# Kernel optimization log

Measured on AMD Instinct MI355X. Metric: run time of the kernel, lower is better.

## Reference

```python
import jax, jax.numpy as jnp
import numpy as np

V, D, H, L = 32000, 1024, 1024, 2
B, S = 64, 256

def setup_inputs() -> dict:
    key = jax.random.key(0)
    k_emb, k_wx, k_wh, k_in, k_len = jax.random.split(key, 5)
    sc = 1.0 / np.sqrt(H)
    embedding = jax.random.normal(k_emb, (V, D), dtype=jnp.float32) * sc
    Wx = jax.random.normal(k_wx, (L, D, 4 * H), dtype=jnp.float32) * sc  # layer input kernels (D==H)
    Wh = jax.random.normal(k_wh, (L, H, 4 * H), dtype=jnp.float32) * sc  # recurrent kernels
    b = jnp.zeros((L, 4 * H), dtype=jnp.float32).at[:, H:2 * H].set(1.0)  # forget-gate bias = 1
    inputs = jax.random.randint(k_in, (B, S), 0, V)
    lengths = jax.random.randint(k_len, (B,), 1, S + 1)
    return {"inputs": inputs, "lengths": lengths, "train": 1,
            "embedding": embedding, "Wx": Wx, "Wh": Wh, "b": b}

def _lstm_layer(x, lengths, Wx, Wh, b):
    # x: [B, S, D]; masked update freezes (c, h) once t >= length (state after EOS).
    Bn, Sn, _ = x.shape
    Hn = Wh.shape[0]
    c0 = jnp.zeros((Bn, Hn), x.dtype)
    h0 = jnp.zeros((Bn, Hn), x.dtype)
    xg = jnp.einsum('bsd,dg->sbg', x, Wx) + b  # precompute input projections [S,B,4H]

    def step(carry, inp):
        c, h, t = carry
        gates = inp + h @ Wh  # [B, 4H]
        i, f, g, o = jnp.split(gates, 4, axis=-1)
        c_new = jax.nn.sigmoid(f) * c + jax.nn.sigmoid(i) * jnp.tanh(g)
        h_new = jax.nn.sigmoid(o) * jnp.tanh(c_new)
        mask = (t < lengths)[:, None]
        c = jnp.where(mask, c_new, c)
        h = jnp.where(mask, h_new, h)
        return (c, h, t + 1), h

    (c_f, h_f, _), hs = jax.lax.scan(step, (c0, h0, jnp.int32(0)), xg)
    return jnp.transpose(hs, (1, 0, 2)), c_f, h_f  # [B,S,H], [B,H], [B,H]

def reference(inputs, lengths, train, embedding, Wx, Wh, b):
    # embed (dropout rates are 0 -> identity)
    x = embedding[inputs]  # [B, S, D]
    cs, hs = [], []
    for l in range(Wx.shape[0]):
        x, c_f, h_f = _lstm_layer(x, lengths, Wx[l], Wh[l], b[l])
        cs.append(c_f)
        hs.append(h_f)
    return x, (jnp.stack(cs), jnp.stack(hs))  # outputs, per-layer final (c, h)
```

## Files before the change

### kernel.cpp

```cpp
#include <hip/hip_runtime.h>
#include <cstdint>
#include <cstddef>

#define VV  32000
#define DD  1024
#define HH  1024
#define LL  2
#define BB  64
#define SS  256
#define G4  4096

typedef __attribute__((ext_vector_type(8))) short short8;
typedef __attribute__((ext_vector_type(4))) float f32x4;
typedef unsigned short u16;
typedef unsigned int u32;

__device__ __forceinline__ u16 f2bf(float f) {
  union { float f; u32 u; } v; v.f = f;
  u32 u = v.u + 0x7fffu + ((v.u >> 16) & 1u);
  return (u16)(u >> 16);
}
__device__ __forceinline__ float bf2f(u16 b) {
  union { u32 u; float f; } v; v.u = ((u32)b) << 16;
  return v.f;
}
__device__ __forceinline__ float sigm(float x) { return 1.f / (1.f + __expf(-x)); }
__device__ __forceinline__ float tanh_fast(float x) {
  return 1.f - 2.f / (__expf(2.f * x) + 1.f);
}

__global__ void embed_kernel(const int* __restrict__ inputs,
                             const float* __restrict__ emb,
                             u16* __restrict__ x0) {
  int m = blockIdx.x;
  int s = m >> 6, b = m & 63;
  int tok = inputs[b * SS + s];
  const f32x4* src = (const f32x4*)(emb + (size_t)tok * DD);
  f32x4 v = src[threadIdx.x];
  u32 lo = (u32)f2bf(v[0]) | ((u32)f2bf(v[1]) << 16);
  u32 hi = (u32)f2bf(v[2]) | ((u32)f2bf(v[3]) << 16);
  u32* dst = (u32*)(x0 + (size_t)m * DD + threadIdx.x * 4);
  dst[0] = lo; dst[1] = hi;
}

__global__ void permW_kernel(const float* __restrict__ Wx, const float* __restrict__ Wh,
                             u16* __restrict__ WxPT, u16* __restrict__ WhPT) {
  __shared__ float tl[64][65];
  int bid = blockIdx.x;
  int which = bid >> 10;
  int tile = bid & 1023;
  int ktile = tile >> 6, ntile = tile & 63;
  const float* src = ((which < 2) ? Wx : Wh) + (size_t)(which & 1) * G4 * 1024;
  u16* dst = ((which < 2) ? WxPT : WhPT) + (size_t)(which & 1) * G4 * 1024;
  int tid = threadIdx.x;
  #pragma unroll
  for (int i = 0; i < 16; ++i) {
    int idx = i * 256 + tid;
    int kk = idx >> 6, nn = idx & 63;
    tl[kk][nn] = src[(size_t)(ktile * 64 + kk) * G4 + ntile * 64 + nn];
  }
  __syncthreads();
  #pragma unroll
  for (int i = 0; i < 16; ++i) {
    int idx = i * 256 + tid;
    int nn = idx >> 6, kk = idx & 63;
    int n = ntile * 64 + nn;
    int p = ((n & 1023) << 2) | (n >> 10);
    dst[(size_t)p * 1024 + ktile * 64 + kk] = f2bf(tl[kk][nn]);
  }
}

__global__ void permB_kernel(const float* __restrict__ bb, float* __restrict__ bP) {
  int idx = blockIdx.x * 256 + threadIdx.x;
  int l = idx >> 12, p = idx & 4095;
  int h = p >> 2, g = p & 3;
  bP[idx] = bb[l * G4 + g * 1024 + h];
}

__device__ __forceinline__ void gld_lds16(const void* g, void* l) {
  __builtin_amdgcn_global_load_lds((const __attribute__((address_space(1))) unsigned int*)g,
                                   (__attribute__((address_space(3))) unsigned int*)l, 16, 0, 0);
}

__global__ __launch_bounds__(256) void gemm_xg(
    const u16* __restrict__ A, const u16* __restrict__ W,
    const float* __restrict__ bP, float* Cf, u16* Cb, int out_f32) {
  __shared__ u16 As[128 * 32];
  __shared__ u16 Bs[128 * 32];
  const int tid = threadIdx.x;
  const int wave = tid >> 6, lane = tid & 63;
  const int bid = blockIdx.x;
  const int nt = bid & 31, mt = bid >> 5;
  const u16* Ap = A + (size_t)mt * 128 * 1024;
  const u16* Wp = W + (size_t)nt * 128 * 1024;
  f32x4 acc[4][4];
  #pragma unroll
  for (int i = 0; i < 4; ++i)
    #pragma unroll
    for (int j = 0; j < 4; ++j) acc[i][j] = (f32x4){0.f, 0.f, 0.f, 0.f};
  const int wm = wave >> 1, wn = wave & 1;
  const int r16 = lane & 15, oct = lane >> 4;
  for (int k0 = 0; k0 < 1024; k0 += 32) {
    #pragma unroll
    for (int issue = 0; issue < 2; ++issue) {
      int cb = issue * 256 + wave * 64;
      int c = cb + lane;
      gld_lds16(Ap + (size_t)(c >> 2) * 1024 + k0 + (c & 3) * 8, As + (size_t)cb * 8);
      gld_lds16(Wp + (size_t)(c >> 2) * 1024 + k0 + (c & 3) * 8, Bs + (size_t)cb * 8);
    }
    asm volatile("s_waitcnt vmcnt(0)" ::: "memory");
    __syncthreads();
    short8 af[4], bfr[4];
    #pragma unroll
    for (int i = 0; i < 4; ++i)
      af[i] = *(const short8*)(As + (wm * 64 + i * 16 + r16) * 32 + oct * 8);
    #pragma unroll
    for (int j = 0; j < 4; ++j)
      bfr[j] = *(const short8*)(Bs + (wn * 64 + j * 16 + r16) * 32 + oct * 8);
    #pragma unroll
    for (int i = 0; i < 4; ++i)
      #pragma unroll
      for (int j = 0; j < 4; ++j)
        acc[i][j] = __builtin_amdgcn_mfma_f32_16x16x32_bf16(af[i], bfr[j], acc[i][j], 0, 0, 0);
    __syncthreads();
  }
  #pragma unroll
  for (int j = 0; j < 4; ++j) {
    int n = nt * 128 + wn * 64 + j * 16 + r16;
    float bias = bP[n];
    #pragma unroll
    for (int i = 0; i < 4; ++i) {
      int m = mt * 128 + wm * 64 + i * 16 + oct * 4;
      #pragma unroll
      for (int r = 0; r < 4; ++r) {
        float val = acc[i][j][r] + bias;
        if (out_f32) Cf[(size_t)(m + r) * G4 + n] = val;
        else         Cb[(size_t)(m + r) * G4 + n] = f2bf(val);
      }
    }
  }
}

__global__ __launch_bounds__(256, 1) void recur_kernel(
    const u16* __restrict__ WhPT,
    const float* xgf, const u16* xgb, int xg_f32,
    const int* __restrict__ lengths,
    u16* __restrict__ hbuf,
    u16* __restrict__ hs_out,
    float* __restrict__ x_out,
    float* __restrict__ c_out, float* __restrict__ h_out,
    int layer, int* flags) {
  __shared__ u16 hA[16][1032];
  __shared__ float gbuf[16][64];
  __shared__ float xgbuf[16][64];
  __shared__ int len_s[16];
  const int tid = threadIdx.x;
  const int wave = tid >> 6, lane = tid & 63;
  const int bg = blockIdx.x >> 6, cg = blockIdx.x & 63;
  const int r16 = lane & 15, oct = lane >> 4;

  short8 bfrag[32];
  {
    const u16* wrow = WhPT + (size_t)(cg * 64 + wave * 16 + r16) * 1024 + oct * 8;
    #pragma unroll
    for (int kk = 0; kk < 32; ++kk) bfrag[kk] = *(const short8*)(wrow + kk * 32);
    #pragma unroll
    for (int kk = 0; kk < 32; ++kk) asm volatile("" : "+a"(bfrag[kk]));
  }
  if (tid < 16) len_s[tid] = lengths[bg * 16 + tid];
  const int b_loc = tid >> 4, hc_loc = tid & 15;
  const int b_glob = bg * 16 + b_loc;
  const int hc_glob = cg * 16 + hc_loc;
  float c_reg = 0.f, h_reg = 0.f;
  if (!(tid & 1))
    __hip_atomic_store((u32*)(hbuf + (size_t)b_glob * 1024 + hc_glob), 0u,
                       __ATOMIC_RELAXED, __HIP_MEMORY_SCOPE_AGENT);

  int* myflags = flags + bg * 64;
  f32x4 xg_next;
  {
    size_t xrow = (size_t)(0 * 64 + b_glob) * G4 + cg * 64 + hc_loc * 4;
    if (xg_f32) xg_next = *(const f32x4*)(xgf + xrow);
    else {
      const u16* s = xgb + xrow;
      f32x4 v; v[0] = bf2f(s[0]); v[1] = bf2f(s[1]); v[2] = bf2f(s[2]); v[3] = bf2f(s[3]);
      xg_next = v;
    }
  }

  for (int t = 0; t < SS; ++t) {
    __syncthreads();
    if (tid == 0)
      __hip_atomic_store(&myflags[cg], t + 1, __ATOMIC_RELAXED, __HIP_MEMORY_SCOPE_AGENT);
    if (wave == 0) {
      while (__hip_atomic_load(&myflags[lane], __ATOMIC_RELAXED, __HIP_MEMORY_SCOPE_AGENT) < t + 1)
        __builtin_amdgcn_s_sleep(1);
    }
    __syncthreads();
    {
      const u16* hsrc = hbuf + (size_t)(t & 1) * (BB * 1024) + (size_t)b_glob * 1024;
      unsigned long long addr = (unsigned long long)(hsrc + hc_loc * 8);
      short8 v0, v1, v2, v3, v4, v5, v6, v7;
      asm volatile(
        "global_load_dwordx4 %0, %8, off sc1\n\t"
        "global_load_dwordx4 %1, %8, off offset:256 sc1\n\t"
        "global_load_dwordx4 %2, %8, off offset:512 sc1\n\t"
        "global_load_dwordx4 %3, %8, off offset:768 sc1\n\t"
        "global_load_dwordx4 %4, %8, off offset:1024 sc1\n\t"
        "global_load_dwordx4 %5, %8, off offset:1280 sc1\n\t"
        "global_load_dwordx4 %6, %8, off offset:1536 sc1\n\t"
        "global_load_dwordx4 %7, %8, off offset:1792 sc1\n\t"
        "s_waitcnt vmcnt(0)"
        : "=v"(v0), "=v"(v1), "=v"(v2), "=v"(v3),
          "=v"(v4), "=v"(v5), "=v"(v6), "=v"(v7)
        : "v"(addr) : "memory");
      *(short8*)(&hA[b_loc][(hc_loc +   0) * 8]) = v0;
      *(short8*)(&hA[b_loc][(hc_loc +  16) * 8]) = v1;
      *(short8*)(&hA[b_loc][(hc_loc +  32) * 8]) = v2;
      *(short8*)(&hA[b_loc][(hc_loc +  48) * 8]) = v3;
      *(short8*)(&hA[b_loc][(hc_loc +  64) * 8]) = v4;
      *(short8*)(&hA[b_loc][(hc_loc +  80) * 8]) = v5;
      *(short8*)(&hA[b_loc][(hc_loc +  96) * 8]) = v6;
      *(short8*)(&hA[b_loc][(hc_loc + 112) * 8]) = v7;
      *(f32x4*)(&xgbuf[b_loc][hc_loc * 4]) = xg_next;
      if (t + 1 < SS) {
        size_t xrow = (size_t)((t + 1) * 64 + b_glob) * G4 + cg * 64 + hc_loc * 4;
        if (xg_f32) xg_next = *(const f32x4*)(xgf + xrow);
        else {
          const u16* s = xgb + xrow;
          f32x4 v; v[0] = bf2f(s[0]); v[1] = bf2f(s[1]); v[2] = bf2f(s[2]); v[3] = bf2f(s[3]);
          xg_next = v;
        }
      }
    }
    __syncthreads();
    f32x4 acc0 = (f32x4){0.f, 0.f, 0.f, 0.f};
    f32x4 acc1 = (f32x4){0.f, 0.f, 0.f, 0.f};
    #pragma unroll
    for (int kk = 0; kk < 16; ++kk) {
      short8 a0 = *(const short8*)(&hA[r16][(2 * kk) * 32 + oct * 8]);
      short8 a1 = *(const short8*)(&hA[r16][(2 * kk + 1) * 32 + oct * 8]);
      acc0 = __builtin_amdgcn_mfma_f32_16x16x32_bf16(a0, bfrag[2 * kk], acc0, 0, 0, 0);
      acc1 = __builtin_amdgcn_mfma_f32_16x16x32_bf16(a1, bfrag[2 * kk + 1], acc1, 0, 0, 0);
    }
    f32x4 acc = acc0 + acc1;
    #pragma unroll
    for (int r = 0; r < 4; ++r) gbuf[oct * 4 + r][wave * 16 + r16] = acc[r];
    __syncthreads();
    f32x4 g = *(const f32x4*)(&gbuf[b_loc][hc_loc * 4]);
    f32x4 xv = *(const f32x4*)(&xgbuf[b_loc][hc_loc * 4]);
    float si = sigm(g[0] + xv[0]);
    float sf = sigm(g[1] + xv[1]);
    float gg = tanh_fast(g[2] + xv[2]);
    float so = sigm(g[3] + xv[3]);
    float c_new = sf * c_reg + si * gg;
    float h_new = so * tanh_fast(c_new);
    if (t < len_s[b_loc]) { c_reg = c_new; h_reg = h_new; }
    u32 hb = (u32)f2bf(h_reg);
    u32 nb = (u32)__shfl_xor((int)hb, 1);
    u32 packed = hb | (nb << 16);
    if (!(tid & 1))
      __hip_atomic_store((u32*)(hbuf + (size_t)((t + 1) & 1) * (BB * 1024) +
                                (size_t)b_glob * 1024 + hc_glob),
                         packed, __ATOMIC_RELAXED, __HIP_MEMORY_SCOPE_AGENT);
    if (layer == 0) {
      if (!(tid & 1))
        __builtin_nontemporal_store(packed,
            (u32*)(hs_out + (size_t)(t * 64 + b_glob) * 1024 + hc_glob));
    } else {
      __builtin_nontemporal_store(h_reg,
          x_out + (size_t)(b_glob * SS + t) * 1024 + hc_glob);
    }
  }
  c_out[(size_t)b_glob * 1024 + hc_glob] = c_reg;
  h_out[(size_t)b_glob * 1024 + hc_glob] = h_reg;
}

extern "C" void kernel_launch(void* const* d_in, const int* in_sizes, int n_in,
                              void* d_out, int out_size, void* d_ws, size_t ws_size,
                              hipStream_t stream) {
  const int* inputs  = (const int*)d_in[0];
  const int* lengths = (const int*)d_in[1];
  const float* emb   = (const float*)d_in[3];
  const float* Wx    = (const float*)d_in[4];
  const float* Wh    = (const float*)d_in[5];
  const float* bb    = (const float*)d_in[6];
  float* out = (float*)d_out;

  char* ws = (char*)d_ws;
  size_t off = 0;
  auto alloc = [&](size_t bytes) -> void* {
    void* p = ws + off;
    off = (off + bytes + 255) & ~(size_t)255;
    return p;
  };
  u16* WxPT = (u16*)alloc((size_t)2 * G4 * 1024 * 2);
  u16* WhPT = (u16*)alloc((size_t)2 * G4 * 1024 * 2);
  float* bP = (float*)alloc((size_t)2 * G4 * 4);
  u16* x0   = (u16*)alloc((size_t)16384 * 1024 * 2);
  u16* hs0  = (u16*)alloc((size_t)16384 * 1024 * 2);
  u16* hbuf = (u16*)alloc((size_t)2 * BB * 1024 * 2);
  int* flags = (int*)alloc(2048);
  size_t xg_f32_bytes = (size_t)16384 * G4 * 4;
  int xg_f32 = (ws_size > off) && ((ws_size - off) >= xg_f32_bytes);
  float* xgf = (float*)(ws + off);
  u16* xgb   = (u16*)(ws + off);

  hipMemsetAsync(flags, 0, 2048, stream);
  embed_kernel<<<dim3(16384), dim3(256), 0, stream>>>(inputs, emb, x0);
  permW_kernel<<<dim3(4096), dim3(256), 0, stream>>>(Wx, Wh, WxPT, WhPT);
  permB_kernel<<<dim3(32), dim3(256), 0, stream>>>(bb, bP);

  float* cs_base = out + (size_t)BB * SS * HH;
  float* hs_base = cs_base + (size_t)LL * BB * HH;

  for (int layer = 0; layer < 2; ++layer) {
    const u16* Aten = (layer == 0) ? x0 : hs0;
    gemm_xg<<<dim3(4096), dim3(256), 0, stream>>>(
        Aten, WxPT + (size_t)layer * G4 * 1024, bP + layer * G4, xgf, xgb, xg_f32);
    const u16* Whl = WhPT + (size_t)layer * G4 * 1024;
    float* c_out_p = cs_base + (size_t)layer * BB * HH;
    float* h_out_p = hs_base + (size_t)layer * BB * HH;
    int* flags_l = flags + layer * 256;
    const float* xgf_c = xgf; const u16* xgb_c = xgb;
    void* args[] = { (void*)&Whl, (void*)&xgf_c, (void*)&xgb_c, (void*)&xg_f32,
                     (void*)&lengths, (void*)&hbuf, (void*)&hs0, (void*)&out,
                     (void*)&c_out_p, (void*)&h_out_p, (void*)&layer,
                     (void*)&flags_l };
    hipLaunchCooperativeKernel((void*)recur_kernel, dim3(256), dim3(256), args, 0, stream);
  }
}
```

Before: 2.765 ms.

## Fuse both LSTM layers into one wavefront-pipelined recurrent kernel

Replaces the two sequential per-layer recurrent kernels, and the layer-1 input-projection GEMM, with one cooperative kernel of 512 threads per block. Waves 0-3 run layer 0 at step s while waves 4-7 run layer 1 at step s-1. Layer 1 computes its input projection on the fly from the layer-0 hidden state, using register-resident Wx1 and Wh1 fragments. This removes one full grid-synchronised sequence of 256 steps, the layer-1 xg GEMM and the hs0 round trip through memory. The cost is double the register pressure for weight fragments, extra MFMA work per step on the layer-1 waves, and one extra step in the pipeline.

```diff
diff --git a/kernel.cpp b/kernel.cpp
--- a/kernel.cpp
+++ b/kernel.cpp
@@ -141,45 +141,89 @@
   }
 }
 
-__global__ __launch_bounds__(256, 1) void recur_kernel(
-    const u16* __restrict__ WhPT,
+#define STAGE_TILE(HSRC, HADST) do {                                          \
+    unsigned long long addr_ = (unsigned long long)((HSRC) + hc_loc * 8);     \
+    short8 v0, v1, v2, v3, v4, v5, v6, v7;                                    \
+    asm volatile(                                                             \
+      "global_load_dwordx4 %0, %8, off sc1\n\t"                               \
+      "global_load_dwordx4 %1, %8, off offset:256 sc1\n\t"                    \
+      "global_load_dwordx4 %2, %8, off offset:512 sc1\n\t"                    \
+      "global_load_dwordx4 %3, %8, off offset:768 sc1\n\t"                    \
+      "global_load_dwordx4 %4, %8, off offset:1024 sc1\n\t"                   \
+      "global_load_dwordx4 %5, %8, off offset:1280 sc1\n\t"                   \
+      "global_load_dwordx4 %6, %8, off offset:1536 sc1\n\t"                   \
+      "global_load_dwordx4 %7, %8, off offset:1792 sc1\n\t"                   \
+      "s_waitcnt vmcnt(0)"                                                    \
+      : "=v"(v0), "=v"(v1), "=v"(v2), "=v"(v3),                               \
+        "=v"(v4), "=v"(v5), "=v"(v6), "=v"(v7)                                \
+      : "v"(addr_) : "memory");                                               \
+    *(short8*)(&(HADST)[b_loc][(hc_loc +   0) * 8]) = v0;                     \
+    *(short8*)(&(HADST)[b_loc][(hc_loc +  16) * 8]) = v1;                     \
+    *(short8*)(&(HADST)[b_loc][(hc_loc +  32) * 8]) = v2;                     \
+    *(short8*)(&(HADST)[b_loc][(hc_loc +  48) * 8]) = v3;                     \
+    *(short8*)(&(HADST)[b_loc][(hc_loc +  64) * 8]) = v4;                     \
+    *(short8*)(&(HADST)[b_loc][(hc_loc +  80) * 8]) = v5;                     \
+    *(short8*)(&(HADST)[b_loc][(hc_loc +  96) * 8]) = v6;                     \
+    *(short8*)(&(HADST)[b_loc][(hc_loc + 112) * 8]) = v7;                     \
+  } while (0)
+
+__global__ __launch_bounds__(512, 1) void recur2_kernel(
+    const u16* __restrict__ Wh0PT,
+    const u16* __restrict__ Wx1PT,
+    const u16* __restrict__ Wh1PT,
     const float* xgf, const u16* xgb, int xg_f32,
+    const float* __restrict__ b1P,
     const int* __restrict__ lengths,
-    u16* __restrict__ hbuf,
-    u16* __restrict__ hs_out,
+    u16* __restrict__ h0buf,
+    u16* __restrict__ h1buf,
     float* __restrict__ x_out,
-    float* __restrict__ c_out, float* __restrict__ h_out,
-    int layer, int* flags) {
-  __shared__ u16 hA[16][1032];
-  __shared__ float gbuf[16][64];
+    float* __restrict__ c0_out, float* __restrict__ h0_out,
+    float* __restrict__ c1_out, float* __restrict__ h1_out,
+    int* flags) {
+  __shared__ u16 hA0[16][1032];
+  __shared__ u16 hA1[16][1032];
+  __shared__ float gbuf0[16][64];
+  __shared__ float gbuf1[16][64];
   __shared__ float xgbuf[16][64];
   __shared__ int len_s[16];
   const int tid = threadIdx.x;
   const int wave = tid >> 6, lane = tid & 63;
   const int bg = blockIdx.x >> 6, cg = blockIdx.x & 63;
   const int r16 = lane & 15, oct = lane >> 4;
-
-  short8 bfrag[32];
+  const bool lo = (wave < 4);
+  const int wv = wave & 3;
+
+  short8 bfA[32], bfB[32];
   {
-    const u16* wrow = WhPT + (size_t)(cg * 64 + wave * 16 + r16) * 1024 + oct * 8;
-    #pragma unroll
-    for (int kk = 0; kk < 32; ++kk) bfrag[kk] = *(const short8*)(wrow + kk * 32);
-    #pragma unroll
-    for (int kk = 0; kk < 32; ++kk) asm volatile("" : "+a"(bfrag[kk]));
+    const u16* rowA = (lo ? Wh0PT : Wx1PT) + (size_t)(cg * 64 + wv * 16 + r16) * 1024 + oct * 8;
+    const u16* rowB = (lo ? Wh0PT : Wh1PT) + (size_t)(cg * 64 + wv * 16 + r16) * 1024 + oct * 8;
+    #pragma unroll
+    for (int kk = 0; kk < 32; ++kk) bfA[kk] = *(const short8*)(rowA + kk * 32);
+    #pragma unroll
+    for (int kk = 0; kk < 32; ++kk) asm volatile("" : "+a"(bfA[kk]));
+    #pragma unroll
+    for (int kk = 0; kk < 32; ++kk) bfB[kk] = *(const short8*)(rowB + kk * 32);
+    #pragma unroll
+    for (int kk = 0; kk < 32; ++kk) asm volatile("" : "+a"(bfB[kk]));
   }
   if (tid < 16) len_s[tid] = lengths[bg * 16 + tid];
-  const int b_loc = tid >> 4, hc_loc = tid & 15;
+  const int th = tid & 255;
+  const int b_loc = th >> 4, hc_loc = th & 15;
   const int b_glob = bg * 16 + b_loc;
   const int hc_glob = cg * 16 + hc_loc;
   float c_reg = 0.f, h_reg = 0.f;
-  if (!(tid & 1))
-    __hip_atomic_store((u32*)(hbuf + (size_t)b_glob * 1024 + hc_glob), 0u,
+  if (!(tid & 1)) {
+    u16* zb = lo ? h0buf : h1buf;
+    __hip_atomic_store((u32*)(zb + (size_t)b_glob * 1024 + hc_glob), 0u,
                        __ATOMIC_RELAXED, __HIP_MEMORY_SCOPE_AGENT);
+  }
+  f32x4 bias1 = (f32x4){0.f, 0.f, 0.f, 0.f};
+  if (!lo) bias1 = *(const f32x4*)(b1P + hc_glob * 4);
 
   int* myflags = flags + bg * 64;
-  f32x4 xg_next;
-  {
-    size_t xrow = (size_t)(0 * 64 + b_glob) * G4 + cg * 64 + hc_loc * 4;
+  f32x4 xg_next = (f32x4){0.f, 0.f, 0.f, 0.f};
+  if (lo) {
+    size_t xrow = (size_t)b_glob * G4 + cg * 64 + hc_loc * 4;
     if (xg_f32) xg_next = *(const f32x4*)(xgf + xrow);
     else {
       const u16* s = xgb + xrow;
@@ -188,92 +232,115 @@
     }
   }
 
-  for (int t = 0; t < SS; ++t) {
+  for (int s = 0; s <= SS; ++s) {
     __syncthreads();
     if (tid == 0)
-      __hip_atomic_store(&myflags[cg], t + 1, __ATOMIC_RELAXED, __HIP_MEMORY_SCOPE_AGENT);
+      __hip_atomic_store(&myflags[cg], s + 1, __ATOMIC_RELAXED, __HIP_MEMORY_SCOPE_AGENT);
     if (wave == 0) {
-      while (__hip_atomic_load(&myflags[lane], __ATOMIC_RELAXED, __HIP_MEMORY_SCOPE_AGENT) < t + 1)
+      while (__hip_atomic_load(&myflags[lane], __ATOMIC_RELAXED, __HIP_MEMORY_SCOPE_AGENT) < s + 1)
         __builtin_amdgcn_s_sleep(1);
     }
     __syncthreads();
-    {
-      const u16* hsrc = hbuf + (size_t)(t & 1) * (BB * 1024) + (size_t)b_glob * 1024;
-      unsigned long long addr = (unsigned long long)(hsrc + hc_loc * 8);
-      short8 v0, v1, v2, v3, v4, v5, v6, v7;
-      asm volatile(
-        "global_load_dwordx4 %0, %8, off sc1\n\t"
-        "global_load_dwordx4 %1, %8, off offset:256 sc1\n\t"
-        "global_load_dwordx4 %2, %8, off offset:512 sc1\n\t"
-        "global_load_dwordx4 %3, %8, off offset:768 sc1\n\t"
-        "global_load_dwordx4 %4, %8, off offset:1024 sc1\n\t"
-        "global_load_dwordx4 %5, %8, off offset:1280 sc1\n\t"
-        "global_load_dwordx4 %6, %8, off offset:1536 sc1\n\t"
-        "global_load_dwordx4 %7, %8, off offset:1792 sc1\n\t"
-        "s_waitcnt vmcnt(0)"
-        : "=v"(v0), "=v"(v1), "=v"(v2), "=v"(v3),
-          "=v"(v4), "=v"(v5), "=v"(v6), "=v"(v7)
-        : "v"(addr) : "memory");
-      *(short8*)(&hA[b_loc][(hc_loc +   0) * 8]) = v0;
-      *(short8*)(&hA[b_loc][(hc_loc +  16) * 8]) = v1;
-      *(short8*)(&hA[b_loc][(hc_loc +  32) * 8]) = v2;
-      *(short8*)(&hA[b_loc][(hc_loc +  48) * 8]) = v3;
-      *(short8*)(&hA[b_loc][(hc_loc +  64) * 8]) = v4;
-      *(short8*)(&hA[b_loc][(hc_loc +  80) * 8]) = v5;
-      *(short8*)(&hA[b_loc][(hc_loc +  96) * 8]) = v6;
-      *(short8*)(&hA[b_loc][(hc_loc + 112) * 8]) = v7;
+    if (lo) {
+      const u16* hsrc = h0buf + (size_t)(s & 1) * (BB * 1024) + (size_t)b_glob * 1024;
+      STAGE_TILE(hsrc, hA0);
       *(f32x4*)(&xgbuf[b_loc][hc_loc * 4]) = xg_next;
-      if (t + 1 < SS) {
-        size_t xrow = (size_t)((t + 1) * 64 + b_glob) * G4 + cg * 64 + hc_loc * 4;
+      if (s + 1 < SS) {
+        size_t xrow = (size_t)((s + 1) * 64 + b_glob) * G4 + cg * 64 + hc_loc * 4;
         if (xg_f32) xg_next = *(const f32x4*)(xgf + xrow);
         else {
-          const u16* s = xgb + xrow;
-          f32x4 v; v[0] = bf2f(s[0]); v[1] = bf2f(s[1]); v[2] = bf2f(s[2]); v[3] = bf2f(s[3]);
+          const u16* sp = xgb + xrow;
+          f32x4 v; v[0] = bf2f(sp[0]); v[1] = bf2f(sp[1]); v[2] = bf2f(sp[2]); v[3] = bf2f(sp[3]);
           xg_next = v;
         }
       }
-    }
-    __syncthreads();
-    f32x4 acc0 = (f32x4){0.f, 0.f, 0.f, 0.f};
-    f32x4 acc1 = (f32x4){0.f, 0.f, 0.f, 0.f};
-    #pragma unroll
-    for (int kk = 0; kk < 16; ++kk) {
-      short8 a0 = *(const short8*)(&hA[r16][(2 * kk) * 32 + oct * 8]);
-      short8 a1 = *(const short8*)(&hA[r16][(2 * kk + 1) * 32 + oct * 8]);
-      acc0 = __builtin_amdgcn_mfma_f32_16x16x32_bf16(a0, bfrag[2 * kk], acc0, 0, 0, 0);
-      acc1 = __builtin_amdgcn_mfma_f32_16x16x32_bf16(a1, bfrag[2 * kk + 1], acc1, 0, 0, 0);
-    }
-    f32x4 acc = acc0 + acc1;
-    #pragma unroll
-    for (int r = 0; r < 4; ++r) gbuf[oct * 4 + r][wave * 16 + r16] = acc[r];
-    __syncthreads();
-    f32x4 g = *(const f32x4*)(&gbuf[b_loc][hc_loc * 4]);
-    f32x4 xv = *(const f32x4*)(&xgbuf[b_loc][hc_loc * 4]);
-    float si = sigm(g[0] + xv[0]);
-    float sf = sigm(g[1] + xv[1]);
-    float gg = tanh_fast(g[2] + xv[2]);
-    float so = sigm(g[3] + xv[3]);
-    float c_new = sf * c_reg + si * gg;
-    float h_new = so * tanh_fast(c_new);
-    if (t < len_s[b_loc]) { c_reg = c_new; h_reg = h_new; }
-    u32 hb = (u32)f2bf(h_reg);
-    u32 nb = (u32)__shfl_xor((int)hb, 1);
-    u32 packed = hb | (nb << 16);
-    if (!(tid & 1))
-      __hip_atomic_store((u32*)(hbuf + (size_t)((t + 1) & 1) * (BB * 1024) +
-                                (size_t)b_glob * 1024 + hc_glob),
-                         packed, __ATOMIC_RELAXED, __HIP_MEMORY_SCOPE_AGENT);
-    if (layer == 0) {
+    } else if (s >= 1) {
+      const u16* hsrc = h1buf + (size_t)((s - 1) & 1) * (BB * 1024) + (size_t)b_glob * 1024;
+      STAGE_TILE(hsrc, hA1);
+    }
+    __syncthreads();
+    if (lo) {
+      if (s < SS) {
+        f32x4 acc0 = (f32x4){0.f, 0.f, 0.f, 0.f};
+        f32x4 acc1 = (f32x4){0.f, 0.f, 0.f, 0.f};
+        #pragma unroll
+        for (int kk = 0; kk < 16; ++kk) {
+          short8 a0 = *(const short8*)(&hA0[r16][(2 * kk) * 32 + oct * 8]);
+          short8 a1 = *(const short8*)(&hA0[r16][(2 * kk + 1) * 32 + oct * 8]);
+          acc0 = __builtin_amdgcn_mfma_f32_16x16x32_bf16(a0, bfA[2 * kk], acc0, 0, 0, 0);
+          acc1 = __builtin_amdgcn_mfma_f32_16x16x32_bf16(a1, bfA[2 * kk + 1], acc1, 0, 0, 0);
+        }
+        f32x4 acc = acc0 + acc1;
+        #pragma unroll
+        for (int r = 0; r < 4; ++r) gbuf0[oct * 4 + r][wv * 16 + r16] = acc[r];
+      }
+    } else if (s >= 1) {
+      f32x4 ax0 = (f32x4){0.f, 0.f, 0.f, 0.f};
+      f32x4 ax1 = (f32x4){0.f, 0.f, 0.f, 0.f};
+      f32x4 ah0 = (f32x4){0.f, 0.f, 0.f, 0.f};
+      f32x4 ah1 = (f32x4){0.f, 0.f, 0.f, 0.f};
+      #pragma unroll
+      for (int kk = 0; kk < 16; ++kk) {
+        short8 a0 = *(const short8*)(&hA0[r16][(2 * kk) * 32 + oct * 8]);
+        short8 a1 = *(const short8*)(&hA0[r16][(2 * kk + 1) * 32 + oct * 8]);
+        short8 c0 = *(const short8*)(&hA1[r16][(2 * kk) * 32 + oct * 8]);
+        short8 c1 = *(const short8*)(&hA1[r16][(2 * kk + 1) * 32 + oct * 8]);
+        ax0 = __builtin_amdgcn_mfma_f32_16x16x32_bf16(a0, bfA[2 * kk], ax0, 0, 0, 0);
+        ax1 = __builtin_amdgcn_mfma_f32_16x16x32_bf16(a1, bfA[2 * kk + 1], ax1, 0, 0, 0);
+        ah0 = __builtin_amdgcn_mfma_f32_16x16x32_bf16(c0, bfB[2 * kk], ah0, 0, 0, 0);
+        ah1 = __builtin_amdgcn_mfma_f32_16x16x32_bf16(c1, bfB[2 * kk + 1], ah1, 0, 0, 0);
+      }
+      f32x4 acc = (ax0 + ax1) + (ah0 + ah1);
+      #pragma unroll
+      for (int r = 0; r < 4; ++r) gbuf1[oct * 4 + r][wv * 16 + r16] = acc[r];
+    }
+    __syncthreads();
+    if (lo) {
+      if (s < SS) {
+        f32x4 g = *(const f32x4*)(&gbuf0[b_loc][hc_loc * 4]);
+        f32x4 xv = *(const f32x4*)(&xgbuf[b_loc][hc_loc * 4]);
+        float si = sigm(g[0] + xv[0]);
+        float sf = sigm(g[1] + xv[1]);
+        float gg = tanh_fast(g[2] + xv[2]);
+        float so = sigm(g[3] + xv[3]);
+        float c_new = sf * c_reg + si * gg;
+        float h_new = so * tanh_fast(c_new);
+        if (s < len_s[b_loc]) { c_reg = c_new; h_reg = h_new; }
+        u32 hb = (u32)f2bf(h_reg);
+        u32 nb = (u32)__shfl_xor((int)hb, 1);
+        u32 packed = hb | (nb << 16);
+        if (!(tid & 1))
+          __hip_atomic_store((u32*)(h0buf + (size_t)((s + 1) & 1) * (BB * 1024) +
+                                    (size_t)b_glob * 1024 + hc_glob),
+                             packed, __ATOMIC_RELAXED, __HIP_MEMORY_SCOPE_AGENT);
+      }
+    } else if (s >= 1) {
+      f32x4 g = *(const f32x4*)(&gbuf1[b_loc][hc_loc * 4]);
+      float si = sigm(g[0] + bias1[0]);
+      float sf = sigm(g[1] + bias1[1]);
+      float gg = tanh_fast(g[2] + bias1[2]);
+      float so = sigm(g[3] + bias1[3]);
+      float c_new = sf * c_reg + si * gg;
+      float h_new = so * tanh_fast(c_new);
+      if (s - 1 < len_s[b_loc]) { c_reg = c_new; h_reg = h_new; }
+      u32 hb = (u32)f2bf(h_reg);
+      u32 nb = (u32)__shfl_xor((int)hb, 1);
+      u32 packed = hb | (nb << 16);
       if (!(tid & 1))
-        __builtin_nontemporal_store(packed,
-            (u32*)(hs_out + (size_t)(t * 64 + b_glob) * 1024 + hc_glob));
-    } else {
+        __hip_atomic_store((u32*)(h1buf + (size_t)(s & 1) * (BB * 1024) +
+                                  (size_t)b_glob * 1024 + hc_glob),
+                           packed, __ATOMIC_RELAXED, __HIP_MEMORY_SCOPE_AGENT);
       __builtin_nontemporal_store(h_reg,
-          x_out + (size_t)(b_glob * SS + t) * 1024 + hc_glob);
-    }
-  }
-  c_out[(size_t)b_glob * 1024 + hc_glob] = c_reg;
-  h_out[(size_t)b_glob * 1024 + hc_glob] = h_reg;
+          x_out + (size_t)(b_glob * SS + (s - 1)) * 1024 + hc_glob);
+    }
+  }
+  if (lo) {
+    c0_out[(size_t)b_glob * 1024 + hc_glob] = c_reg;
+    h0_out[(size_t)b_glob * 1024 + hc_glob] = h_reg;
+  } else {
+    c1_out[(size_t)b_glob * 1024 + hc_glob] = c_reg;
+    h1_out[(size_t)b_glob * 1024 + hc_glob] = h_reg;
+  }
 }
 
 extern "C" void kernel_launch(void* const* d_in, const int* in_sizes, int n_in,
@@ -298,35 +365,40 @@
   u16* WhPT = (u16*)alloc((size_t)2 * G4 * 1024 * 2);
   float* bP = (float*)alloc((size_t)2 * G4 * 4);
   u16* x0   = (u16*)alloc((size_t)16384 * 1024 * 2);
-  u16* hs0  = (u16*)alloc((size_t)16384 * 1024 * 2);
-  u16* hbuf = (u16*)alloc((size_t)2 * BB * 1024 * 2);
-  int* flags = (int*)alloc(2048);
+  u16* h0buf = (u16*)alloc((size_t)2 * BB * 1024 * 2);
+  u16* h1buf = (u16*)alloc((size_t)2 * BB * 1024 * 2);
+  int* flags = (int*)alloc(1024);
   size_t xg_f32_bytes = (size_t)16384 * G4 * 4;
   int xg_f32 = (ws_size > off) && ((ws_size - off) >= xg_f32_bytes);
   float* xgf = (float*)(ws + off);
   u16* xgb   = (u16*)(ws + off);
 
-  hipMemsetAsync(flags, 0, 2048, stream);
+  hipMemsetAsync(flags, 0, 1024, stream);
   embed_kernel<<<dim3(16384), dim3(256), 0, stream>>>(inputs, emb, x0);
   permW_kernel<<<dim3(4096), dim3(256), 0, stream>>>(Wx, Wh, WxPT, WhPT);
   permB_kernel<<<dim3(32), dim3(256), 0, stream>>>(bb, bP);
 
+  gemm_xg<<<dim3(4096), dim3(256), 0, stream>>>(x0, WxPT, bP, xgf, xgb, xg_f32);
+
   float* cs_base = out + (size_t)BB * SS * HH;
   float* hs_base = cs_base + (size_t)LL * BB * HH;
 
-  for (int layer = 0; layer < 2; ++layer) {
-    const u16* Aten = (layer == 0) ? x0 : hs0;
-    gemm_xg<<<dim3(4096), dim3(256), 0, stream>>>(
-        Aten, WxPT + (size_t)layer * G4 * 1024, bP + layer * G4, xgf, xgb, xg_f32);
-    const u16* Whl = WhPT + (size_t)layer * G4 * 1024;
-    float* c_out_p = cs_base + (size_t)layer * BB * HH;
-    float* h_out_p = hs_base + (size_t)layer * BB * HH;
-    int* flags_l = flags + layer * 256;
-    const float* xgf_c = xgf; const u16* xgb_c = xgb;
-    void* args[] = { (void*)&Whl, (void*)&xgf_c, (void*)&xgb_c, (void*)&xg_f32,
-                     (void*)&lengths, (void*)&hbuf, (void*)&hs0, (void*)&out,
-                     (void*)&c_out_p, (void*)&h_out_p, (void*)&layer,
-                     (void*)&flags_l };
-    hipLaunchCooperativeKernel((void*)recur_kernel, dim3(256), dim3(256), args, 0, stream);
-  }
-}
+  const u16* Wh0 = WhPT;
+  const u16* Wx1 = WxPT + (size_t)G4 * 1024;
+  const u16* Wh1 = WhPT + (size_t)G4 * 1024;
+  const float* b1 = bP + G4;
+  const float* xgf_c = xgf;
+  const u16* xgb_c = xgb;
+  float* c0_out = cs_base;
+  float* c1_out = cs_base + (size_t)BB * HH;
+  float* h0_out = hs_base;
+  float* h1_out = hs_base + (size_t)BB * HH;
+  void* args[] = { (void*)&Wh0, (void*)&Wx1, (void*)&Wh1,
+                   (void*)&xgf_c, (void*)&xgb_c, (void*)&xg_f32,
+                   (void*)&b1, (void*)&lengths,
+                   (void*)&h0buf, (void*)&h1buf, (void*)&out,
+                   (void*)&c0_out, (void*)&h0_out,
+                   (void*)&c1_out, (void*)&h1_out,
+                   (void*)&flags };
+  hipLaunchCooperativeKernel((void*)recur2_kernel, dim3(256), dim3(512), args, 0, stream);
+}
```

Result: slower. 3.590 ms (+29.9%).
